# Performance work log

Measured on AMD Instinct MI355X. Metric: run time of the kernel, lower is better.

## Reference

```python
import jax, jax.numpy as jnp
import numpy as np


def _perm_mats():
    E = np.zeros((36, 9), np.float32)
    D = np.zeros((9, 36), np.float32)
    c = 0
    for i in range(8):
        for j in range(i + 1, 9):
            E[c, i] = 1.0
            E[c, j] = 1.0
            D[i, c] = 1.0
            D[j, c] = 1.0
            c += 1
    assert c == 36
    return E, D


def setup_inputs() -> dict:
    key = jax.random.key(0)
    B = 32768
    # binary candidate mask: [B, 9 digits, 9 rows, 9 cols]
    mask = jnp.round(jax.random.uniform(key, (B, 9, 9, 9), dtype=jnp.float32))
    E, D = _perm_mats()
    return {"mask": mask, "enc": jnp.asarray(E), "dec": jnp.asarray(D)}


def _nn_compare(x, v):
    # NNCompare: triangular bump == 1 exactly when x == v (for integer-valued x)
    return jnp.minimum(jax.nn.relu(x - (v - 1.0)), jax.nn.relu((v + 1.0) - x))


def _nn_and(x, y):
    return jnp.clip(jnp.minimum(x, y), 0.0, 1.0)


def reference(mask, enc, dec):
    B = mask.shape[0]
    # encode_permutations: 1x1 conv 9 -> 36 (pair selection)
    perms = jnp.einsum('oc,bchw->bohw', enc, mask)          # [B,36,9,9]
    perms = _nn_compare(perms, 2.0)                          # cell contains exactly this pair
    # sum_all_permutations: 1x1 conv 36 -> 1, then == 1
    sum_p = _nn_compare(jnp.sum(perms, axis=1, keepdims=True), 1.0)  # [B,1,9,9]
    perms = _nn_and(perms, sum_p)                            # broadcast over 36 channels
    # box downsample: grouped 3x3 stride-3 sum conv
    down = perms.reshape(B, 36, 3, 3, 3, 3).sum(axis=(3, 5))  # [B,36,3,3]
    down = _nn_compare(down, 2.0)                              # exactly two such cells in box
    up = jnp.repeat(jnp.repeat(down, 3, axis=2), 3, axis=3)    # [B,36,9,9]
    up = _nn_and(up, 1.0 - perms)                              # other cells in the box
    # decode_permutations: 1x1 conv 36 -> 9
    erase = jnp.einsum('oc,bchw->bohw', dec, up)               # [B,9,9,9]
    return _nn_and(mask, 1.0 - erase)
```

## Files before the change

### kernel.cpp

```cpp
#include <hip/hip_runtime.h>
#include <stdint.h>


#define NB 8
#define NCELL (NB * 81)
#define NBOX (NB * 9)
#define CPT 3

__global__ __launch_bounds__(256) void sudoku_naked_pair_kernel(
    const float* __restrict__ mask, float* __restrict__ out) {
  __shared__ unsigned short pairm[NCELL];
  __shared__ unsigned short erls[NCELL];

  const int tid = threadIdx.x;
  const size_t base = (size_t)blockIdx.x * (NB * 729);

  uint32_t mycell[CPT];

#pragma unroll
  for (int it = 0; it < CPT; ++it) {
    const int c = tid + it * 256;
    if (c < NCELL) {
      const int b = c / 81, cell = c - b * 81;
      const float* p = mask + base + b * 729 + cell;
      uint32_t m = 0;
#pragma unroll
      for (int d = 0; d < 9; ++d) m |= (p[d * 81] != 0.0f ? 1u : 0u) << d;
      mycell[it] = m;
      pairm[c] = (unsigned short)((__popc(m) == 2) ? m : 0u);
    }
  }
  __syncthreads();

  if (tid < NBOX) {
    const int b = tid / 9, bi = tid - b * 9;
    const int bb = b * 81 + (bi / 3) * 27 + (bi % 3) * 3;
    uint32_t pm[9];
#pragma unroll
    for (int j = 0; j < 3; ++j) {
      pm[3 * j + 0] = pairm[bb + 9 * j + 0];
      pm[3 * j + 1] = pairm[bb + 9 * j + 1];
      pm[3 * j + 2] = pairm[bb + 9 * j + 2];
    }
    bool naked[9];
#pragma unroll
    for (int j = 0; j < 9; ++j) {
      int cnt = 0;
#pragma unroll
      for (int k = 0; k < 9; ++k) cnt += (pm[k] == pm[j]);
      naked[j] = (pm[j] != 0u) && (cnt == 2);
    }
#pragma unroll
    for (int j = 0; j < 9; ++j) {
      uint32_t er = 0;
#pragma unroll
      for (int k = 0; k < 9; ++k)
        if (naked[k] && pm[k] != pm[j]) er |= pm[k];
      const int cell = bb + 9 * (j / 3) + (j % 3);
      erls[cell] = (unsigned short)er;
    }
  }
  __syncthreads();

#pragma unroll
  for (int it = 0; it < CPT; ++it) {
    const int c = tid + it * 256;
    if (c < NCELL) {
      const int b = c / 81, cell = c - b * 81;
      const uint32_t fin = mycell[it] & ~(uint32_t)erls[c];
      float* q = out + base + b * 729 + cell;
#pragma unroll
      for (int d = 0; d < 9; ++d) q[d * 81] = (float)((fin >> d) & 1u);
    }
  }
}

extern "C" void kernel_launch(void* const* d_in, const int* in_sizes, int n_in,
                              void* d_out, int out_size, void* d_ws, size_t ws_size,
                              hipStream_t stream) {
  const float* mask = (const float*)d_in[0];
  float* out = (float*)d_out;
  const int B = in_sizes[0] / 729;
  const int grid = B / NB;
  sudoku_naked_pair_kernel<<<grid, 256, 0, stream>>>(mask, out);
}
```

Before: 174.6 us.

## Stage mask through LDS as bytes with float4 global loads and stores

Replaces the per-cell strided scalar loads and stores (stride 81 floats across digits) with contiguous float4 loads into a byte-per-element shared-memory buffer. The per-box threads then gather their cells' digit bits from LDS, apply the naked-pair elimination in place, and write the bytes back, after which all threads emit float4 stores. Batch per block doubles to 16 puzzles. The aim is fully coalesced, vectorized global traffic for a memory-bound kernel, at the cost of byte-granular LDS accesses that may bank-conflict and more serial work in the 144 box threads.

```diff
diff --git a/kernel.cpp b/kernel.cpp
--- a/kernel.cpp
+++ b/kernel.cpp
@@ -2,76 +2,88 @@
 #include <stdint.h>
 
 
-#define NB 8
-#define NCELL (NB * 81)
+#define NB 16
+#define ELEMS (NB * 729)
+#define NWORDS (ELEMS / 4)
 #define NBOX (NB * 9)
-#define CPT 3
 
 __global__ __launch_bounds__(256) void sudoku_naked_pair_kernel(
     const float* __restrict__ mask, float* __restrict__ out) {
-  __shared__ unsigned short pairm[NCELL];
-  __shared__ unsigned short erls[NCELL];
+  __shared__ uint32_t lds32[NWORDS];
+  uint8_t* lds8 = (uint8_t*)lds32;
 
   const int tid = threadIdx.x;
-  const size_t base = (size_t)blockIdx.x * (NB * 729);
+  const size_t base = (size_t)blockIdx.x * ELEMS;
 
-  uint32_t mycell[CPT];
-
-#pragma unroll
-  for (int it = 0; it < CPT; ++it) {
-    const int c = tid + it * 256;
-    if (c < NCELL) {
-      const int b = c / 81, cell = c - b * 81;
-      const float* p = mask + base + b * 729 + cell;
-      uint32_t m = 0;
-#pragma unroll
-      for (int d = 0; d < 9; ++d) m |= (p[d * 81] != 0.0f ? 1u : 0u) << d;
-      mycell[it] = m;
-      pairm[c] = (unsigned short)((__popc(m) == 2) ? m : 0u);
-    }
+  const float4* in4 = (const float4*)(mask + base);
+  for (int i = tid; i < NWORDS; i += 256) {
+    float4 v = in4[i];
+    lds32[i] = (uint32_t)(v.x != 0.0f)
+             | ((uint32_t)(v.y != 0.0f) << 8)
+             | ((uint32_t)(v.z != 0.0f) << 16)
+             | ((uint32_t)(v.w != 0.0f) << 24);
   }
   __syncthreads();
 
   if (tid < NBOX) {
     const int b = tid / 9, bi = tid - b * 9;
-    const int bb = b * 81 + (bi / 3) * 27 + (bi % 3) * 3;
-    uint32_t pm[9];
+    const int boxbase = b * 729 + (bi / 3) * 27 + (bi % 3) * 3;
+
+    uint32_t cellm[9] = {0, 0, 0, 0, 0, 0, 0, 0, 0};
 #pragma unroll
-    for (int j = 0; j < 3; ++j) {
-      pm[3 * j + 0] = pairm[bb + 9 * j + 0];
-      pm[3 * j + 1] = pairm[bb + 9 * j + 1];
-      pm[3 * j + 2] = pairm[bb + 9 * j + 2];
+    for (int d = 0; d < 9; ++d) {
+      const uint8_t* p = lds8 + boxbase + d * 81;
+#pragma unroll
+      for (int r = 0; r < 3; ++r)
+#pragma unroll
+        for (int c = 0; c < 3; ++c)
+          cellm[r * 3 + c] |= ((uint32_t)p[r * 9 + c] & 1u) << d;
     }
+
+    uint32_t pairm[9];
+#pragma unroll
+    for (int j = 0; j < 9; ++j)
+      pairm[j] = (__popc(cellm[j]) == 2) ? cellm[j] : 0u;
+
     bool naked[9];
 #pragma unroll
     for (int j = 0; j < 9; ++j) {
       int cnt = 0;
 #pragma unroll
-      for (int k = 0; k < 9; ++k) cnt += (pm[k] == pm[j]);
-      naked[j] = (pm[j] != 0u) && (cnt == 2);
+      for (int k = 0; k < 9; ++k) cnt += (pairm[k] == pairm[j]);
+      naked[j] = (pairm[j] != 0u) && (cnt == 2);
     }
+
 #pragma unroll
     for (int j = 0; j < 9; ++j) {
       uint32_t er = 0;
 #pragma unroll
       for (int k = 0; k < 9; ++k)
-        if (naked[k] && pm[k] != pm[j]) er |= pm[k];
-      const int cell = bb + 9 * (j / 3) + (j % 3);
-      erls[cell] = (unsigned short)er;
+        if (naked[k] && pairm[k] != pairm[j]) er |= pairm[k];
+      cellm[j] &= ~er;
+    }
+
+#pragma unroll
+    for (int d = 0; d < 9; ++d) {
+      uint8_t* p = lds8 + boxbase + d * 81;
+#pragma unroll
+      for (int r = 0; r < 3; ++r)
+#pragma unroll
+        for (int c = 0; c < 3; ++c)
+          p[r * 9 + c] = (uint8_t)((cellm[r * 3 + c] >> d) & 1u);
     }
   }
   __syncthreads();
 
-#pragma unroll
-  for (int it = 0; it < CPT; ++it) {
-    const int c = tid + it * 256;
-    if (c < NCELL) {
-      const int b = c / 81, cell = c - b * 81;
-      const uint32_t fin = mycell[it] & ~(uint32_t)erls[c];
-      float* q = out + base + b * 729 + cell;
-#pragma unroll
-      for (int d = 0; d < 9; ++d) q[d * 81] = (float)((fin >> d) & 1u);
-    }
+  float4* out4 = (float4*)(out + base);
+  for (int i = tid; i < NWORDS; i += 256) {
+    uint32_t w = lds32[i];
+    float4 v;
+    v.x = (float)(w & 0xFFu);
+    v.y = (float)((w >> 8) & 0xFFu);
+    v.z = (float)((w >> 16) & 0xFFu);
+    v.w = (float)(w >> 24);
+    out4[i] = v;
   }
 }
 
```

After: 183.5 us. 1.05x slower.
